# Performance work log

Hardware: AMD Instinct MI355X
Metric: run time of the kernel (lower is better)

## Reference

```python
import jax, jax.numpy as jnp
import numpy as np

B, Q, D, H, HD = 16, 300, 256, 8, 32
LV, P, NL, FF, NC = 3, 4, 6, 1024, 80
SPATIAL = ((80, 80), (40, 40), (20, 20))
LEN = sum(h * w for h, w in SPATIAL)  # 8400


def _layer_norm(x, g, b):
    m = jnp.mean(x, -1, keepdims=True)
    v = jnp.mean((x - m) ** 2, -1, keepdims=True)
    return (x - m) * jax.lax.rsqrt(v + 1e-5) * g + b


def _inverse_sigmoid(x, eps=1e-5):
    x = jnp.clip(x, eps, 1.0 - eps)
    return jnp.log(x / (1.0 - x))


def _bilinear(img, x, y, Hl, Wl):
    # img: (B*H, C, Hl*Wl); x, y: (B*H, N) pixel coords; matches
    # F.grid_sample(align_corners=False, padding_mode='zeros')
    x0 = jnp.floor(x)
    y0 = jnp.floor(y)
    wx1 = x - x0
    wy1 = y - y0

    def g(xi, yi, w):
        valid = (xi >= 0) & (xi <= Wl - 1) & (yi >= 0) & (yi <= Hl - 1)
        idx = jnp.clip(yi, 0, Hl - 1).astype(jnp.int32) * Wl + jnp.clip(xi, 0, Wl - 1).astype(jnp.int32)
        idxb = jnp.broadcast_to(idx[:, None, :], (img.shape[0], img.shape[1], idx.shape[-1]))
        v = jnp.take_along_axis(img, idxb, axis=2)
        return v * (w * valid)[:, None, :]

    return (g(x0, y0, (1 - wx1) * (1 - wy1)) + g(x0 + 1, y0, wx1 * (1 - wy1))
            + g(x0, y0 + 1, (1 - wx1) * wy1) + g(x0 + 1, y0 + 1, wx1 * wy1))


def _msda(query, ref, value, oW, ob, aW, ab, OW, Ob):
    # query: (B,Q,D); ref: (B,Q,4) in [0,1]; value: (B,LEN,H,HD)
    off = (query @ oW + ob).reshape(B, Q, H, LV, P, 2)
    aw = jax.nn.softmax((query @ aW + ab).reshape(B, Q, H, LV * P), -1).reshape(B, Q, H, LV, P)
    loc = ref[:, :, None, None, None, :2] + off / P * ref[:, :, None, None, None, 2:] * 0.5
    out = jnp.zeros((B, Q, H, HD), query.dtype)
    start = 0
    for l, (Hl, Wl) in enumerate(SPATIAL):
        img = value[:, start:start + Hl * Wl].transpose(0, 2, 3, 1).reshape(B * H, HD, Hl * Wl)
        start += Hl * Wl
        gl = loc[:, :, :, l].transpose(0, 2, 1, 3, 4).reshape(B * H, Q * P, 2)
        s = _bilinear(img, gl[..., 0] * Wl - 0.5, gl[..., 1] * Hl - 0.5, Hl, Wl).reshape(B, H, HD, Q, P)
        out = out + jnp.einsum('bhdqp,bqhp->bqhd', s, aw[:, :, :, l])
    return out.reshape(B, Q, D) @ OW + Ob


def _mha(qx, kx, vx, Wq, bq, Wk, bk, Wv, bv, Wo, bo):
    q = (qx @ Wq + bq).reshape(B, Q, H, HD)
    k = (kx @ Wk + bk).reshape(B, Q, H, HD)
    v = (vx @ Wv + bv).reshape(B, Q, H, HD)
    a = jax.nn.softmax(jnp.einsum('bqhd,bkhd->bhqk', q, k) * np.float32(1.0 / np.sqrt(HD)), -1)
    return jnp.einsum('bhqk,bkhd->bqhd', a, v).reshape(B, Q, D) @ Wo + bo


def _core(tgt, ref_points_unact, memory, self_Wq, self_bq, self_Wk, self_bk, self_Wv, self_bv, self_Wo, self_bo, ln1_g, ln1_b, ln2_g, ln2_b, ln3_g, ln3_b, off_W, off_b, aw_W, aw_b, val_W, val_b, out_W, out_b, ffn_W1, ffn_b1, ffn_W2, ffn_b2, qph_W1, qph_b1, qph_W2, qph_b2, bb_W1, bb_b1, bb_W2, bb_b2, bb_W3, bb_b3, sc_W, sc_b):
    out = tgt
    ref = jax.nn.sigmoid(ref_points_unact)
    for i in range(NL):
        qpe = jax.nn.relu(ref @ qph_W1 + qph_b1) @ qph_W2 + qph_b2
        q = out + qpe
        out = _layer_norm(out + _mha(q, q, out, self_Wq[i], self_bq[i], self_Wk[i], self_bk[i], self_Wv[i], self_bv[i], self_Wo[i], self_bo[i]), ln1_g[i], ln1_b[i])
        value = (memory @ val_W[i] + val_b[i]).reshape(B, LEN, H, HD)
        out = _layer_norm(out + _msda(out + qpe, ref, value, off_W[i], off_b[i], aw_W[i], aw_b[i], out_W[i], out_b[i]), ln2_g[i], ln2_b[i])
        ff = jax.nn.relu(out @ ffn_W1[i] + ffn_b1[i]) @ ffn_W2[i] + ffn_b2[i]
        out = _layer_norm(out + ff, ln3_g[i], ln3_b[i])
        bb = jax.nn.relu(out @ bb_W1[i] + bb_b1[i])
        bb = jax.nn.relu(bb @ bb_W2[i] + bb_b2[i])
        bb = bb @ bb_W3[i] + bb_b3[i]
        ref = jax.nn.sigmoid(bb + _inverse_sigmoid(ref))
    logits = out @ sc_W[NL - 1] + sc_b[NL - 1]
    return ref, logits


def setup_inputs():
    ks = iter(jax.random.split(jax.random.key(0), 48))

    def rn(shape, s=0.02):
        return jax.random.normal(next(ks), shape, jnp.float32) * s

    z = lambda shape: jnp.zeros(shape, jnp.float32)
    o = lambda shape: jnp.ones(shape, jnp.float32)
    L = NL
    return {
        'tgt': rn((B, Q, D), 1.0),
        'ref_points_unact': rn((B, Q, 4), 1.0),
        'memory': rn((B, LEN, D), 1.0),
        'memory_spatial_shapes': jnp.array(SPATIAL, jnp.int32),
        'self_Wq': rn((L, D, D)), 'self_bq': z((L, D)),
        'self_Wk': rn((L, D, D)), 'self_bk': z((L, D)),
        'self_Wv': rn((L, D, D)), 'self_bv': z((L, D)),
        'self_Wo': rn((L, D, D)), 'self_bo': z((L, D)),
        'ln1_g': o((L, D)), 'ln1_b': z((L, D)),
        'ln2_g': o((L, D)), 'ln2_b': z((L, D)),
        'ln3_g': o((L, D)), 'ln3_b': z((L, D)),
        'off_W': rn((L, D, H * LV * P * 2)), 'off_b': rn((L, H * LV * P * 2), 0.5),
        'aw_W': rn((L, D, H * LV * P)), 'aw_b': z((L, H * LV * P)),
        'val_W': rn((L, D, D)), 'val_b': z((L, D)),
        'out_W': rn((L, D, D)), 'out_b': z((L, D)),
        'ffn_W1': rn((L, D, FF)), 'ffn_b1': z((L, FF)),
        'ffn_W2': rn((L, FF, D)), 'ffn_b2': z((L, D)),
        'qph_W1': rn((4, 2 * D)), 'qph_b1': z((2 * D,)),
        'qph_W2': rn((2 * D, D)), 'qph_b2': z((D,)),
        'bb_W1': rn((L, D, D)), 'bb_b1': z((L, D)),
        'bb_W2': rn((L, D, D)), 'bb_b2': z((L, D)),
        'bb_W3': rn((L, D, 4)), 'bb_b3': z((L, 4)),
        'sc_W': rn((L, D, NC)), 'sc_b': z((L, NC)),
    }


def reference(tgt, ref_points_unact, memory, memory_spatial_shapes, self_Wq, self_bq, self_Wk, self_bk, self_Wv, self_bv, self_Wo, self_bo, ln1_g, ln1_b, ln2_g, ln2_b, ln3_g, ln3_b, off_W, off_b, aw_W, aw_b, val_W, val_b, out_W, out_b, ffn_W1, ffn_b1, ffn_W2, ffn_b2, qph_W1, qph_b1, qph_W2, qph_b2, bb_W1, bb_b1, bb_W2, bb_b2, bb_W3, bb_b3, sc_W, sc_b):
    # memory_spatial_shapes must equal SPATIAL (static constants under jit)
    ref, logits = _core(tgt, ref_points_unact, memory, self_Wq, self_bq, self_Wk, self_bk, self_Wv, self_bv, self_Wo, self_bo, ln1_g, ln1_b, ln2_g, ln2_b, ln3_g, ln3_b, off_W, off_b, aw_W, aw_b, val_W, val_b, out_W, out_b, ffn_W1, ffn_b1, ffn_W2, ffn_b2, qph_W1, qph_b1, qph_W2, qph_b2, bb_W1, bb_b1, bb_W2, bb_b2, bb_W3, bb_b3, sc_W, sc_b)
    # eval path: stacked outputs from the eval_idx (last) layer
    return (ref[None], logits[None])
```

## Files before the change

### kernel.cpp

```cpp
#include <hip/hip_runtime.h>

#define DI __device__ __forceinline__

typedef __attribute__((ext_vector_type(8))) short short8;
typedef __attribute__((ext_vector_type(4))) float f32x4;
typedef unsigned short u16;

DI u16 f2bf(float f) {
    union { float f; unsigned u; } v; v.f = f;
    unsigned u = v.u;
    return (u16)((u + 0x7fffu + ((u >> 16) & 1u)) >> 16);
}
DI float bf2f(u16 h) {
    union { unsigned u; float f; } v; v.u = ((unsigned)h) << 16;
    return v.f;
}
DI int lds_off(int row, int slot) {
    return row * 64 + (((slot ^ ((row >> 1) & 3)) << 4));
}

__global__ __launch_bounds__(256) void k_wt(const float* __restrict__ W, u16* __restrict__ Wt,
                                            int K, int N, int dstL)
{
    __shared__ u16 t[32][33];
    const int tid = threadIdx.x;
    const int kt = blockIdx.x * 32, nt = blockIdx.y * 32;
    const float* Wl = W + (size_t)blockIdx.z * K * N;
    u16* Wtl = Wt + (size_t)blockIdx.z * dstL;
#pragma unroll
    for (int i = 0; i < 4; i++) {
        int k = kt + (tid >> 5) + i * 8;
        int n = nt + (tid & 31);
        float v = (n < N) ? Wl[(size_t)k * N + n] : 0.f;
        t[tid & 31][(tid >> 5) + i * 8] = f2bf(v);
    }
    __syncthreads();
#pragma unroll
    for (int i = 0; i < 4; i++) {
        int n = nt + (tid >> 5) + i * 8;
        int k = kt + (tid & 31);
        if (n < N) Wtl[(size_t)n * K + k] = t[(tid >> 5) + i * 8][tid & 31];
    }
}

__global__ void k_packbias(const float* __restrict__ a, const float* __restrict__ b,
                           int na, int nb, float* __restrict__ dst)
{
    int i = blockIdx.x * 256 + threadIdx.x;
    int L = blockIdx.z;
    float* d = dst + (size_t)L * (na + nb);
    if (i < na) d[i] = a[(size_t)L * na + i];
    if (i < nb) d[na + i] = b[(size_t)L * nb + i];
}

template<int TM, int AMODE, int STORE, bool RELU, bool RESID>
__global__ __launch_bounds__(256) void k_gemm(
    const void* __restrict__ Ap, const float* __restrict__ A2,
    const u16* __restrict__ Bt, const float* __restrict__ bias,
    const float* __restrict__ resid, void* __restrict__ Cp,
    int M, int N, int K)
{
    constexpr int MI = TM / 32;
    __shared__ alignas(16) char Asm[TM * 64];
    __shared__ alignas(16) char Bsm[128 * 64];
    const int tid  = threadIdx.x;
    const int lane = tid & 63;
    const int wave = tid >> 6;
    const int wr = wave >> 1, wc = wave & 1;
    const int m0 = blockIdx.x * TM, n0 = blockIdx.y * 128;

    f32x4 acc[MI][4] = {};

    for (int kb = 0; kb < K; kb += 32) {
        if (AMODE == 2) {
            const u16* A = (const u16*)Ap;
            int r = tid >> 2, ko = (tid & 3) << 3;
            int grow = m0 + r; if (grow > M - 1) grow = M - 1;
            uint4 v = *(const uint4*)(A + (size_t)grow * K + kb + ko);
            *(uint4*)(Asm + lds_off(r, ko >> 3)) = v;
        } else {
            constexpr int AIT = (TM * 8) / 256;
#pragma unroll
            for (int j = 0; j < AIT; j++) {
                int flat = tid + j * 256;
                int r = flat >> 3, kq = flat & 7;
                int grow = m0 + r; if (grow > M - 1) grow = M - 1;
                const float* p = (const float*)Ap + (size_t)grow * K + kb + (kq << 2);
                float4 v = *(const float4*)p;
                if (AMODE == 1) {
                    float4 w = *(const float4*)(A2 + (size_t)grow * K + kb + (kq << 2));
                    v.x += w.x; v.y += w.y; v.z += w.z; v.w += w.w;
                }
                ushort4 h; h.x = f2bf(v.x); h.y = f2bf(v.y); h.z = f2bf(v.z); h.w = f2bf(v.w);
                *(ushort4*)(Asm + lds_off(r, kq >> 1) + ((kq & 1) << 3)) = h;
            }
        }
#pragma unroll
        for (int j = 0; j < 2; j++) {
            int item = tid + j * 256;
            int n = item >> 2, kq = item & 3;
            int gn = n0 + n; if (gn > N - 1) gn = N - 1;
            uint4 v = *(const uint4*)(Bt + (size_t)gn * K + kb + (kq << 3));
            *(uint4*)(Bsm + lds_off(n, kq)) = v;
        }
        __syncthreads();

        short8 af[MI], bfr[4];
#pragma unroll
        for (int mi = 0; mi < MI; mi++) {
            int r = wr * (TM / 2) + (mi << 4) + (lane & 15);
            af[mi] = *(const short8*)(Asm + lds_off(r, lane >> 4));
        }
#pragma unroll
        for (int ni = 0; ni < 4; ni++) {
            int c = (wc << 6) + (ni << 4) + (lane & 15);
            bfr[ni] = *(const short8*)(Bsm + lds_off(c, lane >> 4));
        }
#pragma unroll
        for (int mi = 0; mi < MI; mi++)
#pragma unroll
            for (int ni = 0; ni < 4; ni++)
                acc[mi][ni] = __builtin_amdgcn_mfma_f32_16x16x32_bf16(af[mi], bfr[ni], acc[mi][ni], 0, 0, 0);
        __syncthreads();
    }

    const int cl = lane & 15, rb = (lane >> 4) << 2;
#pragma unroll
    for (int mi = 0; mi < MI; mi++) {
#pragma unroll
        for (int ni = 0; ni < 4; ni++) {
            int col = n0 + (wc << 6) + (ni << 4) + cl;
            if (col >= N) continue;
            float bv = bias[col];
#pragma unroll
            for (int e = 0; e < 4; e++) {
                int row = m0 + wr * (TM / 2) + (mi << 4) + rb + e;
                if (row >= M) continue;
                float v = acc[mi][ni][e] + bv;
                if (RESID) v += resid[(size_t)row * N + col];
                if (RELU)  v = fmaxf(v, 0.f);
                if (STORE == 0) {
                    ((float*)Cp)[(size_t)row * N + col] = v;
                } else {
                    int b = row / 8400, pix = row - b * 8400;
                    int h = col >> 5, hd = col & 31;
                    ((u16*)Cp)[(((size_t)(b * 8 + h)) * 8400 + pix) * 32 + hd] = f2bf(v);
                }
            }
        }
    }
}

__global__ __launch_bounds__(256) void k_mha3(const float* __restrict__ qk, const float* __restrict__ Vp,
                                              float* __restrict__ outp)
{
    __shared__ alignas(16) char lds[62976];
    u16* Ksh = (u16*)lds;
    u16* Psh = (u16*)lds;
    u16* Vt  = (u16*)(lds + 41984);

    const int q0 = blockIdx.x * 64;
    const int bh = blockIdx.y;
    const int h = bh & 7, b = bh >> 3;
    const int tid = threadIdx.x;
    const int wv = tid >> 6, l = tid & 63;
    const int c15 = l & 15, slot = l >> 4;
    const float scale = 0.17677669529663687f;

    for (int item = tid; item < 304 * 8; item += 256) {
        int kk = item >> 3, dq = (item & 7) << 2;
        ushort4 hv = {0, 0, 0, 0};
        if (kk < 300) {
            float4 v = *(const float4*)(qk + (size_t)(b * 300 + kk) * 512 + 256 + h * 32 + dq);
            hv.x = f2bf(v.x); hv.y = f2bf(v.y); hv.z = f2bf(v.z); hv.w = f2bf(v.w);
        }
        *(ushort4*)(Ksh + kk * 40 + dq) = hv;
    }
    for (int item = tid; item < 320 * 8; item += 256) {
        int kk = item >> 3, dq = (item & 7) << 2;
        float4 v = {0, 0, 0, 0};
        if (kk < 300)
            v = *(const float4*)(Vp + (size_t)(b * 300 + kk) * 256 + h * 32 + dq);
        Vt[(dq + 0) * 328 + kk] = f2bf(v.x);
        Vt[(dq + 1) * 328 + kk] = f2bf(v.y);
        Vt[(dq + 2) * 328 + kk] = f2bf(v.z);
        Vt[(dq + 3) * 328 + kk] = f2bf(v.w);
    }
    short8 qf;
    {
        int qrow = q0 + 16 * wv + c15; if (qrow > 299) qrow = 299;
        const float* qs = qk + (size_t)(b * 300 + qrow) * 512 + h * 32 + (slot << 3);
        float4 a0 = *(const float4*)qs, a1 = *(const float4*)(qs + 4);
        qf[0] = (short)f2bf(a0.x * scale); qf[1] = (short)f2bf(a0.y * scale);
        qf[2] = (short)f2bf(a0.z * scale); qf[3] = (short)f2bf(a0.w * scale);
        qf[4] = (short)f2bf(a1.x * scale); qf[5] = (short)f2bf(a1.y * scale);
        qf[6] = (short)f2bf(a1.z * scale); qf[7] = (short)f2bf(a1.w * scale);
    }
    __syncthreads();

    f32x4 sc[19];
    const f32x4 zero4 = {0.f, 0.f, 0.f, 0.f};
#pragma unroll
    for (int t = 0; t < 19; t++) {
        short8 kf = *(const short8*)(Ksh + (16 * t + c15) * 40 + (slot << 3));
        sc[t] = __builtin_amdgcn_mfma_f32_16x16x32_bf16(qf, kf, zero4, 0, 0, 0);
    }
    __syncthreads();

    float linv[4];
    const int prow0 = 16 * wv + (slot << 2);
#pragma unroll
    for (int e = 0; e < 4; e++) {
        float mm = -1e30f;
#pragma unroll
        for (int t = 0; t < 18; t++) mm = fmaxf(mm, sc[t][e]);
        if (c15 < 12) mm = fmaxf(mm, sc[18][e]);
        mm = fmaxf(mm, __shfl_xor(mm, 1));
        mm = fmaxf(mm, __shfl_xor(mm, 2));
        mm = fmaxf(mm, __shfl_xor(mm, 4));
        mm = fmaxf(mm, __shfl_xor(mm, 8));
        float ls = 0.f;
#pragma unroll
        for (int t = 0; t < 19; t++) {
            float p = __expf(sc[t][e] - mm);
            if (t == 18 && c15 >= 12) p = 0.f;
            ls += p;
            Psh[(prow0 + e) * 328 + 16 * t + c15] = f2bf(p);
        }
        ls += __shfl_xor(ls, 1);
        ls += __shfl_xor(ls, 2);
        ls += __shfl_xor(ls, 4);
        ls += __shfl_xor(ls, 8);
        linv[e] = 1.f / ls;
    }
    {
        int r = 16 * wv + (l >> 2);
        int c = 304 + ((l & 3) << 2);
        Psh[r * 328 + c + 0] = 0; Psh[r * 328 + c + 1] = 0;
        Psh[r * 328 + c + 2] = 0; Psh[r * 328 + c + 3] = 0;
    }

#pragma unroll
    for (int df = 0; df < 2; df++) {
        f32x4 o = zero4;
#pragma unroll
        for (int t = 0; t < 10; t++) {
            short8 pf = *(const short8*)(Psh + (16 * wv + c15) * 328 + 32 * t + (slot << 3));
            short8 vf = *(const short8*)(Vt + (16 * df + c15) * 328 + 32 * t + (slot << 3));
            o = __builtin_amdgcn_mfma_f32_16x16x32_bf16(pf, vf, o, 0, 0, 0);
        }
#pragma unroll
        for (int e = 0; e < 4; e++) {
            int qrow = q0 + prow0 + e;
            if (qrow < 300)
                outp[(size_t)(b * 300 + qrow) * 256 + h * 32 + 16 * df + c15] = o[e] * linv[e];
        }
    }
}

__global__ __launch_bounds__(256) void k_ln(const float* __restrict__ x, const float* __restrict__ g,
                                            const float* __restrict__ bb, float* __restrict__ out, int M)
{
    int row = blockIdx.x * 4 + (threadIdx.x >> 6);
    int lane = threadIdx.x & 63;
    if (row >= M) return;
    const float* xr = x + (size_t)row * 256;
    float4 v = *(const float4*)(xr + lane * 4);
    float s  = v.x + v.y + v.z + v.w;
    float s2 = v.x*v.x + v.y*v.y + v.z*v.z + v.w*v.w;
#pragma unroll
    for (int off = 32; off >= 1; off >>= 1) {
        s  += __shfl_xor(s, off);
        s2 += __shfl_xor(s2, off);
    }
    float m   = s * 0.00390625f;
    float var = s2 * 0.00390625f - m * m;
    float r   = rsqrtf(var + 1e-5f);
    float4 gv = *(const float4*)(g + lane * 4);
    float4 bv = *(const float4*)(bb + lane * 4);
    float4 o;
    o.x = (v.x - m) * r * gv.x + bv.x;
    o.y = (v.y - m) * r * gv.y + bv.y;
    o.z = (v.z - m) * r * gv.z + bv.z;
    o.w = (v.w - m) * r * gv.w + bv.w;
    *(float4*)(out + (size_t)row * 256 + lane * 4) = o;
}

__global__ void k_awsm(float* __restrict__ offaw, int n)
{
    int g = blockIdx.x * 256 + threadIdx.x;
    if (g >= n) return;
    int row = g >> 3, h = g & 7;
    float* p = offaw + (size_t)row * 288 + 192 + h * 12;
    float m = p[0];
#pragma unroll
    for (int i = 1; i < 12; i++) m = fmaxf(m, p[i]);
    float e[12]; float s = 0.f;
#pragma unroll
    for (int i = 0; i < 12; i++) { e[i] = __expf(p[i] - m); s += e[i]; }
    float inv = 1.f / s;
#pragma unroll
    for (int i = 0; i < 12; i++) p[i] = e[i] * inv;
}

__global__ __launch_bounds__(256) void k_msda(const u16* __restrict__ value, const float* __restrict__ offaw,
                                              const float* __restrict__ ref, float* __restrict__ samp)
{
    int it = blockIdx.x * 8 + (threadIdx.x >> 5);
    int d  = threadIdx.x & 31;
    int h = it & 7, row = it >> 3;
    int b = row / 300;
    const float* rf = ref + (size_t)row * 4;
    float rx = rf[0], ry = rf[1];
    float rw = rf[2] * 0.125f, rh = rf[3] * 0.125f;
    const float* offp = offaw + (size_t)row * 288 + h * 24;
    const float* awp  = offaw + (size_t)row * 288 + 192 + h * 12;
    const u16* vb = value + ((size_t)(b * 8 + h)) * 8400 * 32 + d;
    const int HW[3] = {80, 40, 20};
    const int st[3] = {0, 6400, 8000};
    float acc = 0.f;
#pragma unroll
    for (int lv = 0; lv < 3; lv++) {
        int Wl = HW[lv], Hl = HW[lv];
        float Wf = (float)Wl, Hf = (float)Hl;
#pragma unroll
        for (int p = 0; p < 4; p++) {
            float a = awp[lv * 4 + p];
            float x = (rx + offp[lv*8 + p*2]     * rw) * Wf - 0.5f;
            float y = (ry + offp[lv*8 + p*2 + 1] * rh) * Hf - 0.5f;
            float xf = floorf(x), yf = floorf(y);
            float wx = x - xf, wy = y - yf;
            int x0 = (int)xf, y0 = (int)yf;
#pragma unroll
            for (int t = 0; t < 4; t++) {
                int xx = x0 + (t & 1), yy = y0 + (t >> 1);
                if (xx >= 0 && xx < Wl && yy >= 0 && yy < Hl) {
                    float w = ((t & 1) ? wx : 1.f - wx) * ((t >> 1) ? wy : 1.f - wy);
                    acc += a * w * bf2f(vb[(size_t)(st[lv] + yy * Wl + xx) * 32]);
                }
            }
        }
    }
    samp[(size_t)row * 256 + h * 32 + d] = acc;
}

__global__ void k_qpe_hidden(const float* __restrict__ ref, const float* __restrict__ W1,
                             const float* __restrict__ b1, float* __restrict__ hid)
{
    int idx = blockIdx.x * 256 + threadIdx.x;
    if (idx >= 4800 * 512) return;
    int row = idx >> 9, col = idx & 511;
    const float* r = ref + (size_t)row * 4;
    float v = b1[col] + r[0]*W1[col] + r[1]*W1[512+col] + r[2]*W1[1024+col] + r[3]*W1[1536+col];
    hid[idx] = fmaxf(v, 0.f);
}

__global__ __launch_bounds__(64) void k_bb3(const float* __restrict__ bb2, const float* __restrict__ W3,
                                            const float* __restrict__ b3, float* __restrict__ ref)
{
    int row = blockIdx.x;
    int lane = threadIdx.x;
    const float* xr = bb2 + (size_t)row * 256;
    float s0 = 0, s1 = 0, s2 = 0, s3 = 0;
#pragma unroll
    for (int k = lane; k < 256; k += 64) {
        float xv = xr[k];
        float4 w = *(const float4*)(W3 + k * 4);
        s0 += xv * w.x; s1 += xv * w.y; s2 += xv * w.z; s3 += xv * w.w;
    }
#pragma unroll
    for (int off = 32; off >= 1; off >>= 1) {
        s0 += __shfl_xor(s0, off); s1 += __shfl_xor(s1, off);
        s2 += __shfl_xor(s2, off); s3 += __shfl_xor(s3, off);
    }
    if (lane == 0) {
        float sv[4] = {s0, s1, s2, s3};
        float* rr = ref + (size_t)row * 4;
#pragma unroll
        for (int j = 0; j < 4; j++) {
            float v = sv[j] + b3[j];
            float o = rr[j];
            o = fminf(fmaxf(o, 1e-5f), 1.f - 1e-5f);
            float inv = logf(o / (1.f - o));
            rr[j] = 1.f / (1.f + expf(-(v + inv)));
        }
    }
}

__global__ void k_cvt_bf16(const float* __restrict__ in, u16* __restrict__ out, int n4)
{
    int i = blockIdx.x * 256 + threadIdx.x;
    if (i >= n4) return;
    float4 v = ((const float4*)in)[i];
    ushort4 h; h.x = f2bf(v.x); h.y = f2bf(v.y); h.z = f2bf(v.z); h.w = f2bf(v.w);
    ((ushort4*)out)[i] = h;
}
__global__ void k_copy4(const float* __restrict__ in, float* __restrict__ out, int n4)
{
    int i = blockIdx.x * 256 + threadIdx.x;
    if (i >= n4) return;
    ((float4*)out)[i] = ((const float4*)in)[i];
}
__global__ void k_sigmoid(const float* __restrict__ in, float* __restrict__ out, int n)
{
    int i = blockIdx.x * 256 + threadIdx.x;
    if (i >= n) return;
    out[i] = 1.f / (1.f + __expf(-in[i]));
}

static inline dim3 g32(int M, int N) { return dim3((M + 31) / 32, (N + 127) / 128); }

static void gemm_plain(const float* A, const u16* Bt, const float* bias, float* C,
                       int M, int N, int K, hipStream_t s) {
    k_gemm<32, 0, 0, false, false><<<g32(M, N), 256, 0, s>>>((const void*)A, nullptr, Bt, bias, nullptr, (void*)C, M, N, K);
}
static void gemm_add(const float* A, const float* A2, const u16* Bt, const float* bias, float* C,
                     int M, int N, int K, hipStream_t s) {
    k_gemm<32, 1, 0, false, false><<<g32(M, N), 256, 0, s>>>((const void*)A, A2, Bt, bias, nullptr, (void*)C, M, N, K);
}
static void gemm_resid(const float* A, const u16* Bt, const float* bias, const float* resid, float* C,
                       int M, int N, int K, hipStream_t s) {
    k_gemm<32, 0, 0, false, true><<<g32(M, N), 256, 0, s>>>((const void*)A, nullptr, Bt, bias, resid, (void*)C, M, N, K);
}
static void gemm_relu(const float* A, const u16* Bt, const float* bias, float* C,
                      int M, int N, int K, hipStream_t s) {
    k_gemm<32, 0, 0, true, false><<<g32(M, N), 256, 0, s>>>((const void*)A, nullptr, Bt, bias, nullptr, (void*)C, M, N, K);
}
static void gemm_value(const u16* A, const u16* Bt, const float* bias, u16* C, hipStream_t s) {
    k_gemm<64, 2, 1, false, false><<<dim3(2100, 2), 256, 0, s>>>((const void*)A, nullptr, Bt, bias, nullptr, (void*)C, 134400, 256, 256);
}

extern "C" void kernel_launch(void* const* d_in, const int* in_sizes, int n_in,
                              void* d_out, int out_size, void* d_ws, size_t ws_size,
                              hipStream_t stream)
{
    const float* tgt       = (const float*)d_in[0];
    const float* ref_unact = (const float*)d_in[1];
    const float* memory    = (const float*)d_in[2];
    const float* self_Wq = (const float*)d_in[4];
    const float* self_bq = (const float*)d_in[5];
    const float* self_Wk = (const float*)d_in[6];
    const float* self_bk = (const float*)d_in[7];
    const float* self_Wv = (const float*)d_in[8];
    const float* self_bv = (const float*)d_in[9];
    const float* self_Wo = (const float*)d_in[10];
    const float* self_bo = (const float*)d_in[11];
    const float* ln1_g = (const float*)d_in[12];
    const float* ln1_b = (const float*)d_in[13];
    const float* ln2_g = (const float*)d_in[14];
    const float* ln2_b = (const float*)d_in[15];
    const float* ln3_g = (const float*)d_in[16];
    const float* ln3_b = (const float*)d_in[17];
    const float* off_W = (const float*)d_in[18];
    const float* off_b = (const float*)d_in[19];
    const float* aw_W  = (const float*)d_in[20];
    const float* aw_b  = (const float*)d_in[21];
    const float* val_W = (const float*)d_in[22];
    const float* val_b = (const float*)d_in[23];
    const float* out_W = (const float*)d_in[24];
    const float* out_b = (const float*)d_in[25];
    const float* ffn_W1 = (const float*)d_in[26];
    const float* ffn_b1 = (const float*)d_in[27];
    const float* ffn_W2 = (const float*)d_in[28];
    const float* ffn_b2 = (const float*)d_in[29];
    const float* qph_W1 = (const float*)d_in[30];
    const float* qph_b1 = (const float*)d_in[31];
    const float* qph_W2 = (const float*)d_in[32];
    const float* qph_b2 = (const float*)d_in[33];
    const float* bb_W1 = (const float*)d_in[34];
    const float* bb_b1 = (const float*)d_in[35];
    const float* bb_W2 = (const float*)d_in[36];
    const float* bb_b2 = (const float*)d_in[37];
    const float* bb_W3 = (const float*)d_in[38];
    const float* bb_b3 = (const float*)d_in[39];
    const float* sc_W  = (const float*)d_in[40];
    const float* sc_b  = (const float*)d_in[41];
    float* out_f = (float*)d_out;

    char* w = (char*)d_ws;
    u16* mem_bf = (u16*)(w + 0);
    u16* value  = (u16*)(w + 68812800);
    const size_t F0 = 137625600;
    float* ws_out   = (float*)(w + F0);
    float* ws_tmp   = (float*)(w + F0 +  4915200);
    float* ws_qpe   = (float*)(w + F0 +  9830400);
    float* ws_hid   = (float*)(w + F0 + 14745600);
    float* ws_qk    = (float*)(w + F0 + 24576000);
    float* ws_v     = (float*)(w + F0 + 34406400);
    float* ws_attn  = (float*)(w + F0 + 39321600);
    float* ws_offaw = (float*)(w + F0 + 44236800);
    float* ws_samp  = (float*)(w + F0 + 49766400);
    float* ws_ffn   = (float*)(w + F0 + 54681600);
    float* ws_bb1   = (float*)(w + F0 + 74342400);
    float* ws_bb2   = (float*)(w + F0 + 79257600);
    float* ws_ref   = (float*)(w + F0 + 84172800);
    float* bias_qk  = (float*)(w + F0 + 84256800);
    float* bias_oa  = (float*)(w + F0 + 84269088);
    u16* wt = (u16*)(w + F0 + 84276000);
    u16* wt_qk    = wt;
    u16* wt_v     = wt_qk    + 786432;
    u16* wt_o     = wt_v     + 393216;
    u16* wt_offaw = wt_o     + 393216;
    u16* wt_val   = wt_offaw + 442368;
    u16* wt_out   = wt_val   + 393216;
    u16* wt_f1    = wt_out   + 393216;
    u16* wt_f2    = wt_f1    + 1572864;
    u16* wt_b1    = wt_f2    + 1572864;
    u16* wt_b2    = wt_b1    + 393216;
    u16* wt_qp2   = wt_b2    + 393216;
    u16* wt_sc    = wt_qp2   + 131072;

    k_wt<<<dim3(8, 8, 6),  256, 0, stream>>>(self_Wq, wt_qk,            256, 256, 131072);
    k_wt<<<dim3(8, 8, 6),  256, 0, stream>>>(self_Wk, wt_qk + 65536,    256, 256, 131072);
    k_wt<<<dim3(8, 8, 6),  256, 0, stream>>>(self_Wv, wt_v,             256, 256, 65536);
    k_wt<<<dim3(8, 8, 6),  256, 0, stream>>>(self_Wo, wt_o,             256, 256, 65536);
    k_wt<<<dim3(8, 6, 6),  256, 0, stream>>>(off_W,   wt_offaw,         256, 192, 73728);
    k_wt<<<dim3(8, 3, 6),  256, 0, stream>>>(aw_W,    wt_offaw + 49152, 256, 96,  73728);
    k_wt<<<dim3(8, 8, 6),  256, 0, stream>>>(val_W,   wt_val,           256, 256, 65536);
    k_wt<<<dim3(8, 8, 6),  256, 0, stream>>>(out_W,   wt_out,           256, 256, 65536);
    k_wt<<<dim3(8, 32, 6), 256, 0, stream>>>(ffn_W1,  wt_f1,            256, 1024, 262144);
    k_wt<<<dim3(32, 8, 6), 256, 0, stream>>>(ffn_W2,  wt_f2,            1024, 256, 262144);
    k_wt<<<dim3(8, 8, 6),  256, 0, stream>>>(bb_W1,   wt_b1,            256, 256, 65536);
    k_wt<<<dim3(8, 8, 6),  256, 0, stream>>>(bb_W2,   wt_b2,            256, 256, 65536);
    k_wt<<<dim3(16, 8, 1), 256, 0, stream>>>(qph_W2,  wt_qp2,           512, 256, 131072);
    k_wt<<<dim3(8, 3, 1),  256, 0, stream>>>(sc_W + (size_t)5 * 20480, wt_sc, 256, 80, 20480);
    k_packbias<<<dim3(1, 1, 6), 256, 0, stream>>>(self_bq, self_bk, 256, 256, bias_qk);
    k_packbias<<<dim3(1, 1, 6), 256, 0, stream>>>(off_b, aw_b, 192, 96, bias_oa);

    k_cvt_bf16<<<33600, 256, 0, stream>>>(memory, mem_bf, 8601600);
    k_copy4   <<<1200,  256, 0, stream>>>(tgt, ws_out, 307200);
    k_sigmoid <<<75,    256, 0, stream>>>(ref_unact, ws_ref, 19200);

    for (int l = 0; l < 6; l++) {
        k_qpe_hidden<<<9600, 256, 0, stream>>>(ws_ref, qph_W1, qph_b1, ws_hid);
        gemm_plain(ws_hid, wt_qp2, qph_b2, ws_qpe, 4800, 256, 512, stream);

        gemm_add(ws_out, ws_qpe, wt_qk + (size_t)l * 131072, bias_qk + l * 512, ws_qk, 4800, 512, 256, stream);
        gemm_plain(ws_out, wt_v + (size_t)l * 65536, self_bv + l * 256, ws_v, 4800, 256, 256, stream);
        k_mha3<<<dim3(5, 128), 256, 0, stream>>>(ws_qk, ws_v, ws_attn);
        gemm_resid(ws_attn, wt_o + (size_t)l * 65536, self_bo + l * 256, ws_out, ws_tmp, 4800, 256, 256, stream);
        k_ln<<<1200, 256, 0, stream>>>(ws_tmp, ln1_g + l * 256, ln1_b + l * 256, ws_out, 4800);

        gemm_value(mem_bf, wt_val + (size_t)l * 65536, val_b + l * 256, value, stream);

        gemm_add(ws_out, ws_qpe, wt_offaw + (size_t)l * 73728, bias_oa + l * 288, ws_offaw, 4800, 288, 256, stream);
        k_awsm<<<150, 256, 0, stream>>>(ws_offaw, 38400);
        k_msda<<<4800, 256, 0, stream>>>(value, ws_offaw, ws_ref, ws_samp);
        gemm_resid(ws_samp, wt_out + (size_t)l * 65536, out_b + l * 256, ws_out, ws_tmp, 4800, 256, 256, stream);
        k_ln<<<1200, 256, 0, stream>>>(ws_tmp, ln2_g + l * 256, ln2_b + l * 256, ws_out, 4800);

        gemm_relu(ws_out, wt_f1 + (size_t)l * 262144, ffn_b1 + l * 1024, ws_ffn, 4800, 1024, 256, stream);
        gemm_resid(ws_ffn, wt_f2 + (size_t)l * 262144, ffn_b2 + l * 256, ws_out, ws_tmp, 4800, 256, 1024, stream);
        k_ln<<<1200, 256, 0, stream>>>(ws_tmp, ln3_g + l * 256, ln3_b + l * 256, ws_out, 4800);

        gemm_relu(ws_out, wt_b1 + (size_t)l * 65536, bb_b1 + l * 256, ws_bb1, 4800, 256, 256, stream);
        gemm_relu(ws_bb1, wt_b2 + (size_t)l * 65536, bb_b2 + l * 256, ws_bb2, 4800, 256, 256, stream);
        k_bb3<<<4800, 64, 0, stream>>>(ws_bb2, bb_W3 + (size_t)l * 1024, bb_b3 + l * 4, ws_ref);
    }

    k_copy4<<<19, 256, 0, stream>>>(ws_ref, out_f, 4800);
    gemm_plain(ws_out, wt_sc, sc_b + 5 * 80, out_f + 19200, 4800, 80, 256, stream);
}
```

Baseline: 2.208 ms.

## Fuse QKV projections into one GEMM, fold softmax into MSDA, enlarge value tile

The Q/K and V projections become a single 768-wide GEMM. A new A-mode adds the positional embedding only for the Q/K column blocks, and the attention kernel reads Q, K and V from one buffer. The separate attention-weight softmax kernel is removed and the softmax is computed inside each MSDA thread. The value-projection GEMM moves to a 128-row tile with a loop over A loads. Together these cut per-layer launches and extra passes over memory, at the cost of redundant softmax work per thread and more registers in the larger tile.

Measured after the change: 2.195 ms. Within noise of the previous version (-0.6%).

```diff
diff --git a/kernel.cpp b/kernel.cpp
--- a/kernel.cpp
+++ b/kernel.cpp
@@ -43,14 +43,12 @@
     }
 }
 
-__global__ void k_packbias(const float* __restrict__ a, const float* __restrict__ b,
-                           int na, int nb, float* __restrict__ dst)
+__global__ void k_packb(const float* __restrict__ src, int n, float* __restrict__ dst,
+                        int off, int dstL)
 {
     int i = blockIdx.x * 256 + threadIdx.x;
     int L = blockIdx.z;
-    float* d = dst + (size_t)L * (na + nb);
-    if (i < na) d[i] = a[(size_t)L * na + i];
-    if (i < nb) d[na + i] = b[(size_t)L * nb + i];
+    if (i < n) dst[(size_t)L * dstL + off + i] = src[(size_t)L * n + i];
 }
 
 template<int TM, int AMODE, int STORE, bool RELU, bool RESID>
@@ -68,16 +66,21 @@
     const int wave = tid >> 6;
     const int wr = wave >> 1, wc = wave & 1;
     const int m0 = blockIdx.x * TM, n0 = blockIdx.y * 128;
+    const bool addA2 = (AMODE == 1) || (AMODE == 3 && n0 < 512);
 
     f32x4 acc[MI][4] = {};
 
     for (int kb = 0; kb < K; kb += 32) {
         if (AMODE == 2) {
             const u16* A = (const u16*)Ap;
-            int r = tid >> 2, ko = (tid & 3) << 3;
-            int grow = m0 + r; if (grow > M - 1) grow = M - 1;
-            uint4 v = *(const uint4*)(A + (size_t)grow * K + kb + ko);
-            *(uint4*)(Asm + lds_off(r, ko >> 3)) = v;
+#pragma unroll
+            for (int j = 0; j < (TM * 4) / 256; j++) {
+                int item = tid + j * 256;
+                int r = item >> 2, ko = (item & 3) << 3;
+                int grow = m0 + r; if (grow > M - 1) grow = M - 1;
+                uint4 v = *(const uint4*)(A + (size_t)grow * K + kb + ko);
+                *(uint4*)(Asm + lds_off(r, ko >> 3)) = v;
+            }
         } else {
             constexpr int AIT = (TM * 8) / 256;
 #pragma unroll
@@ -87,7 +90,7 @@
                 int grow = m0 + r; if (grow > M - 1) grow = M - 1;
                 const float* p = (const float*)Ap + (size_t)grow * K + kb + (kq << 2);
                 float4 v = *(const float4*)p;
-                if (AMODE == 1) {
+                if (addA2) {
                     float4 w = *(const float4*)(A2 + (size_t)grow * K + kb + (kq << 2));
                     v.x += w.x; v.y += w.y; v.z += w.z; v.w += w.w;
                 }
@@ -151,8 +154,7 @@
     }
 }
 
-__global__ __launch_bounds__(256) void k_mha3(const float* __restrict__ qk, const float* __restrict__ Vp,
-                                              float* __restrict__ outp)
+__global__ __launch_bounds__(256) void k_mha3(const float* __restrict__ qkv, float* __restrict__ outp)
 {
     __shared__ alignas(16) char lds[62976];
     u16* Ksh = (u16*)lds;
@@ -171,7 +173,7 @@
         int kk = item >> 3, dq = (item & 7) << 2;
         ushort4 hv = {0, 0, 0, 0};
         if (kk < 300) {
-            float4 v = *(const float4*)(qk + (size_t)(b * 300 + kk) * 512 + 256 + h * 32 + dq);
+            float4 v = *(const float4*)(qkv + (size_t)(b * 300 + kk) * 768 + 256 + h * 32 + dq);
             hv.x = f2bf(v.x); hv.y = f2bf(v.y); hv.z = f2bf(v.z); hv.w = f2bf(v.w);
         }
         *(ushort4*)(Ksh + kk * 40 + dq) = hv;
@@ -180,7 +182,7 @@
         int kk = item >> 3, dq = (item & 7) << 2;
         float4 v = {0, 0, 0, 0};
         if (kk < 300)
-            v = *(const float4*)(Vp + (size_t)(b * 300 + kk) * 256 + h * 32 + dq);
+            v = *(const float4*)(qkv + (size_t)(b * 300 + kk) * 768 + 512 + h * 32 + dq);
         Vt[(dq + 0) * 328 + kk] = f2bf(v.x);
         Vt[(dq + 1) * 328 + kk] = f2bf(v.y);
         Vt[(dq + 2) * 328 + kk] = f2bf(v.z);
@@ -189,7 +191,7 @@
     short8 qf;
     {
         int qrow = q0 + 16 * wv + c15; if (qrow > 299) qrow = 299;
-        const float* qs = qk + (size_t)(b * 300 + qrow) * 512 + h * 32 + (slot << 3);
+        const float* qs = qkv + (size_t)(b * 300 + qrow) * 768 + h * 32 + (slot << 3);
         float4 a0 = *(const float4*)qs, a1 = *(const float4*)(qs + 4);
         qf[0] = (short)f2bf(a0.x * scale); qf[1] = (short)f2bf(a0.y * scale);
         qf[2] = (short)f2bf(a0.z * scale); qf[3] = (short)f2bf(a0.w * scale);
@@ -286,23 +288,6 @@
     *(float4*)(out + (size_t)row * 256 + lane * 4) = o;
 }
 
-__global__ void k_awsm(float* __restrict__ offaw, int n)
-{
-    int g = blockIdx.x * 256 + threadIdx.x;
-    if (g >= n) return;
-    int row = g >> 3, h = g & 7;
-    float* p = offaw + (size_t)row * 288 + 192 + h * 12;
-    float m = p[0];
-#pragma unroll
-    for (int i = 1; i < 12; i++) m = fmaxf(m, p[i]);
-    float e[12]; float s = 0.f;
-#pragma unroll
-    for (int i = 0; i < 12; i++) { e[i] = __expf(p[i] - m); s += e[i]; }
-    float inv = 1.f / s;
-#pragma unroll
-    for (int i = 0; i < 12; i++) p[i] = e[i] * inv;
-}
-
 __global__ __launch_bounds__(256) void k_msda(const u16* __restrict__ value, const float* __restrict__ offaw,
                                               const float* __restrict__ ref, float* __restrict__ samp)
 {
@@ -315,6 +300,18 @@
     float rw = rf[2] * 0.125f, rh = rf[3] * 0.125f;
     const float* offp = offaw + (size_t)row * 288 + h * 24;
     const float* awp  = offaw + (size_t)row * 288 + 192 + h * 12;
+    float aw[12];
+    {
+        float mm = awp[0];
+#pragma unroll
+        for (int i = 1; i < 12; i++) mm = fmaxf(mm, awp[i]);
+        float ssum = 0.f;
+#pragma unroll
+        for (int i = 0; i < 12; i++) { aw[i] = __expf(awp[i] - mm); ssum += aw[i]; }
+        float inv = 1.f / ssum;
+#pragma unroll
+        for (int i = 0; i < 12; i++) aw[i] *= inv;
+    }
     const u16* vb = value + ((size_t)(b * 8 + h)) * 8400 * 32 + d;
     const int HW[3] = {80, 40, 20};
     const int st[3] = {0, 6400, 8000};
@@ -325,7 +322,7 @@
         float Wf = (float)Wl, Hf = (float)Hl;
 #pragma unroll
         for (int p = 0; p < 4; p++) {
-            float a = awp[lv * 4 + p];
+            float a = aw[lv * 4 + p];
             float x = (rx + offp[lv*8 + p*2]     * rw) * Wf - 0.5f;
             float y = (ry + offp[lv*8 + p*2 + 1] * rh) * Hf - 0.5f;
             float xf = floorf(x), yf = floorf(y);
@@ -418,6 +415,10 @@
                      int M, int N, int K, hipStream_t s) {
     k_gemm<32, 1, 0, false, false><<<g32(M, N), 256, 0, s>>>((const void*)A, A2, Bt, bias, nullptr, (void*)C, M, N, K);
 }
+static void gemm_qkv(const float* A, const float* A2, const u16* Bt, const float* bias, float* C,
+                     hipStream_t s) {
+    k_gemm<32, 3, 0, false, false><<<g32(4800, 768), 256, 0, s>>>((const void*)A, A2, Bt, bias, nullptr, (void*)C, 4800, 768, 256);
+}
 static void gemm_resid(const float* A, const u16* Bt, const float* bias, const float* resid, float* C,
                        int M, int N, int K, hipStream_t s) {
     k_gemm<32, 0, 0, false, true><<<g32(M, N), 256, 0, s>>>((const void*)A, nullptr, Bt, bias, resid, (void*)C, M, N, K);
@@ -427,7 +428,7 @@
     k_gemm<32, 0, 0, true, false><<<g32(M, N), 256, 0, s>>>((const void*)A, nullptr, Bt, bias, nullptr, (void*)C, M, N, K);
 }
 static void gemm_value(const u16* A, const u16* Bt, const float* bias, u16* C, hipStream_t s) {
-    k_gemm<64, 2, 1, false, false><<<dim3(2100, 2), 256, 0, s>>>((const void*)A, nullptr, Bt, bias, nullptr, (void*)C, 134400, 256, 256);
+    k_gemm<128, 2, 1, false, false><<<dim3(1050, 2), 256, 0, s>>>((const void*)A, nullptr, Bt, bias, nullptr, (void*)C, 134400, 256, 256);
 }
 
 extern "C" void kernel_launch(void* const* d_in, const int* in_sizes, int n_in,
@@ -482,24 +483,21 @@
     u16* value  = (u16*)(w + 68812800);
     const size_t F0 = 137625600;
     float* ws_out   = (float*)(w + F0);
-    float* ws_tmp   = (float*)(w + F0 +  4915200);
-    float* ws_qpe   = (float*)(w + F0 +  9830400);
-    float* ws_hid   = (float*)(w + F0 + 14745600);
-    float* ws_qk    = (float*)(w + F0 + 24576000);
-    float* ws_v     = (float*)(w + F0 + 34406400);
-    float* ws_attn  = (float*)(w + F0 + 39321600);
-    float* ws_offaw = (float*)(w + F0 + 44236800);
-    float* ws_samp  = (float*)(w + F0 + 49766400);
-    float* ws_ffn   = (float*)(w + F0 + 54681600);
-    float* ws_bb1   = (float*)(w + F0 + 74342400);
-    float* ws_bb2   = (float*)(w + F0 + 79257600);
-    float* ws_ref   = (float*)(w + F0 + 84172800);
-    float* bias_qk  = (float*)(w + F0 + 84256800);
-    float* bias_oa  = (float*)(w + F0 + 84269088);
-    u16* wt = (u16*)(w + F0 + 84276000);
-    u16* wt_qk    = wt;
-    u16* wt_v     = wt_qk    + 786432;
-    u16* wt_o     = wt_v     + 393216;
+    float* ws_qpe   = (float*)(w + F0 +  4915200);
+    float* ws_hid   = (float*)(w + F0 +  9830400);
+    float* ws_qkv   = (float*)(w + F0 + 19660800);
+    float* ws_attn  = (float*)(w + F0 + 34406400);
+    float* ws_offaw = (float*)(w + F0 + 39321600);
+    float* ws_samp  = (float*)(w + F0 + 44851200);
+    float* ws_ffn   = (float*)(w + F0 + 49766400);
+    float* ws_bb1   = (float*)(w + F0 + 69427200);
+    float* ws_bb2   = (float*)(w + F0 + 74342400);
+    float* ws_ref   = (float*)(w + F0 + 79257600);
+    float* bias_qkv = (float*)(w + F0 + 79334400);
+    float* bias_oa  = (float*)(w + F0 + 79352832);
+    u16* wt = (u16*)(w + F0 + 79360000);
+    u16* wt_qkv   = wt;
+    u16* wt_o     = wt_qkv   + 1179648;
     u16* wt_offaw = wt_o     + 393216;
     u16* wt_val   = wt_offaw + 442368;
     u16* wt_out   = wt_val   + 393216;
@@ -509,10 +507,11 @@
     u16* wt_b2    = wt_b1    + 393216;
     u16* wt_qp2   = wt_b2    + 393216;
     u16* wt_sc    = wt_qp2   + 131072;
-
-    k_wt<<<dim3(8, 8, 6),  256, 0, stream>>>(self_Wq, wt_qk,            256, 256, 131072);
-    k_wt<<<dim3(8, 8, 6),  256, 0, stream>>>(self_Wk, wt_qk + 65536,    256, 256, 131072);
-    k_wt<<<dim3(8, 8, 6),  256, 0, stream>>>(self_Wv, wt_v,             256, 256, 65536);
+    float* ws_tmp   = (float*)(w + F0 + 79360000 + 13770752);
+
+    k_wt<<<dim3(8, 8, 6),  256, 0, stream>>>(self_Wq, wt_qkv,           256, 256, 196608);
+    k_wt<<<dim3(8, 8, 6),  256, 0, stream>>>(self_Wk, wt_qkv + 65536,   256, 256, 196608);
+    k_wt<<<dim3(8, 8, 6),  256, 0, stream>>>(self_Wv, wt_qkv + 131072,  256, 256, 196608);
     k_wt<<<dim3(8, 8, 6),  256, 0, stream>>>(self_Wo, wt_o,             256, 256, 65536);
     k_wt<<<dim3(8, 6, 6),  256, 0, stream>>>(off_W,   wt_offaw,         256, 192, 73728);
     k_wt<<<dim3(8, 3, 6),  256, 0, stream>>>(aw_W,    wt_offaw + 49152, 256, 96,  73728);
@@ -524,8 +523,11 @@
     k_wt<<<dim3(8, 8, 6),  256, 0, stream>>>(bb_W2,   wt_b2,            256, 256, 65536);
     k_wt<<<dim3(16, 8, 1), 256, 0, stream>>>(qph_W2,  wt_qp2,           512, 256, 131072);
     k_wt<<<dim3(8, 3, 1),  256, 0, stream>>>(sc_W + (size_t)5 * 20480, wt_sc, 256, 80, 20480);
-    k_packbias<<<dim3(1, 1, 6), 256, 0, stream>>>(self_bq, self_bk, 256, 256, bias_qk);
-    k_packbias<<<dim3(1, 1, 6), 256, 0, stream>>>(off_b, aw_b, 192, 96, bias_oa);
+    k_packb<<<dim3(1, 1, 6), 256, 0, stream>>>(self_bq, 256, bias_qkv, 0,   768);
+    k_packb<<<dim3(1, 1, 6), 256, 0, stream>>>(self_bk, 256, bias_qkv, 256, 768);
+    k_packb<<<dim3(1, 1, 6), 256, 0, stream>>>(self_bv, 256, bias_qkv, 512, 768);
+    k_packb<<<dim3(1, 1, 6), 256, 0, stream>>>(off_b,   192, bias_oa,  0,   288);
+    k_packb<<<dim3(1, 1, 6), 256, 0, stream>>>(aw_b,     96, bias_oa,  192, 288);
 
     k_cvt_bf16<<<33600, 256, 0, stream>>>(memory, mem_bf, 8601600);
     k_copy4   <<<1200,  256, 0, stream>>>(tgt, ws_out, 307200);
@@ -535,16 +537,14 @@
         k_qpe_hidden<<<9600, 256, 0, stream>>>(ws_ref, qph_W1, qph_b1, ws_hid);
         gemm_plain(ws_hid, wt_qp2, qph_b2, ws_qpe, 4800, 256, 512, stream);
 
-        gemm_add(ws_out, ws_qpe, wt_qk + (size_t)l * 131072, bias_qk + l * 512, ws_qk, 4800, 512, 256, stream);
-        gemm_plain(ws_out, wt_v + (size_t)l * 65536, self_bv + l * 256, ws_v, 4800, 256, 256, stream);
-        k_mha3<<<dim3(5, 128), 256, 0, stream>>>(ws_qk, ws_v, ws_attn);
+        gemm_qkv(ws_out, ws_qpe, wt_qkv + (size_t)l * 196608, bias_qkv + l * 768, ws_qkv, stream);
+        k_mha3<<<dim3(5, 128), 256, 0, stream>>>(ws_qkv, ws_attn);
         gemm_resid(ws_attn, wt_o + (size_t)l * 65536, self_bo + l * 256, ws_out, ws_tmp, 4800, 256, 256, stream);
         k_ln<<<1200, 256, 0, stream>>>(ws_tmp, ln1_g + l * 256, ln1_b + l * 256, ws_out, 4800);
 
         gemm_value(mem_bf, wt_val + (size_t)l * 65536, val_b + l * 256, value, stream);
 
         gemm_add(ws_out, ws_qpe, wt_offaw + (size_t)l * 73728, bias_oa + l * 288, ws_offaw, 4800, 288, 256, stream);
-        k_awsm<<<150, 256, 0, stream>>>(ws_offaw, 38400);
         k_msda<<<4800, 256, 0, stream>>>(value, ws_offaw, ws_ref, ws_samp);
         gemm_resid(ws_samp, wt_out + (size_t)l * 65536, out_b + l * 256, ws_out, ws_tmp, 4800, 256, 256, stream);
         k_ln<<<1200, 256, 0, stream>>>(ws_tmp, ln2_g + l * 256, ln2_b + l * 256, ws_out, 4800);
```
